# Kernel optimization log

Hardware: AMD Instinct MI355X
Metric: run time of the kernel (lower is better)

Reference implementation:

```python
import jax, jax.numpy as jnp
import numpy as np

S, B, K = 1024, 16, 1024
QD, KD = 1024, 1024


def setup_inputs() -> dict:
    key = jax.random.key(0)
    k1, k2, k3, k4 = jax.random.split(key, 4)
    queries = jax.random.normal(k1, (S, B, QD), dtype=jnp.float32)
    keys = jax.random.normal(k2, (B, K, KD), dtype=jnp.float32)
    null_mask = jax.random.randint(k3, (B, K), 0, 2).astype(jnp.bool_)
    W_in = jax.random.normal(k4, (KD, QD), dtype=jnp.float32) * 0.02
    return {"queries": queries, "keys": keys, "null_mask": null_mask, "W_in": W_in}


def reference(queries, keys, null_mask, W_in):
    # queries: (S, B, QD); keys: (B, K, KD); null_mask: (B, K); W_in: (KD, QD)
    t_query = jnp.einsum('sbq,dq->sbd', queries, W_in)          # linear_in, no bias
    alpha = jnp.einsum('sbd,bkd->sbk', t_query, keys)           # unscaled bilinear scores
    alpha = jnp.where(null_mask[None, :, :], -jnp.inf, alpha)   # masked_fill_
    att_weight = jax.nn.softmax(alpha, axis=2)                  # (S, B, K)
    attened_keys = jnp.einsum('sbk,bkd->sbd', att_weight, keys) # (S, B, KD)
    return (attened_keys, alpha)
```

## Files before the change

### kernel.cpp

```cpp
#include <hip/hip_runtime.h>
#include <math.h>

#define S_DIM 1024
#define B_DIM 16
#define K_DIM 1024
#define QD_DIM 1024
#define KD_DIM 1024
#define MASK_NEG (-3.0e38f)

using short4v = __attribute__((ext_vector_type(4))) short;
using short8v = __attribute__((ext_vector_type(8))) short;
using float4v = __attribute__((ext_vector_type(4))) float;

constexpr int TILE = 128;
constexpr int BK   = 32;
constexpr int LDK  = 36;

#define MFMA(a, b, c) __builtin_amdgcn_mfma_f32_16x16x32_bf16(a, b, c, 0, 0, 0)

__device__ inline void split4(const float4 v, uint2& hi, uint2& lo) {
    uint ax = __float_as_uint(v.x), ay = __float_as_uint(v.y);
    uint az = __float_as_uint(v.z), aw = __float_as_uint(v.w);
    hi.x = __builtin_amdgcn_perm(ay, ax, 0x07060302u);
    hi.y = __builtin_amdgcn_perm(aw, az, 0x07060302u);
    float rx = v.x - __uint_as_float(ax & 0xFFFF0000u);
    float ry = v.y - __uint_as_float(ay & 0xFFFF0000u);
    float rz = v.z - __uint_as_float(az & 0xFFFF0000u);
    float rw = v.w - __uint_as_float(aw & 0xFFFF0000u);
    lo.x = __builtin_amdgcn_perm(__float_as_uint(ry), __float_as_uint(rx), 0x07060302u);
    lo.y = __builtin_amdgcn_perm(__float_as_uint(rw), __float_as_uint(rz), 0x07060302u);
}

__device__ inline short8v frag_load(const short* base) {
    short4v a = *(const short4v*)base;
    short4v b = *(const short4v*)(base + 4);
    return __builtin_shufflevector(a, b, 0, 1, 2, 3, 4, 5, 6, 7);
}

__global__ __launch_bounds__(256) void g1_mfma(const float* __restrict__ Q,
                                               const float* __restrict__ W,
                                               float* __restrict__ TQ) {
    __shared__ short Ah[TILE * LDK], Al[TILE * LDK], Bh[TILE * LDK], Bl[TILE * LDK];
    const int t = threadIdx.x;
    const int lane = t & 63, w = t >> 6;
    const int wm = w >> 1, wn = w & 1;
    const int quad = lane >> 4, l15 = lane & 15;
    const int m0 = blockIdx.y * TILE, n0 = blockIdx.x * TILE;
    const int sr = t >> 3;
    const int sc = (t & 7) * 4;

    float4v acc[4][4] = {};

    for (int k0 = 0; k0 < QD_DIM; k0 += BK) {
        #pragma unroll
        for (int i = 0; i < 4; ++i) {
            const int r = sr + i * 32;
            uint2 h, l;
            float4 va = *(const float4*)(Q + (size_t)(m0 + r) * QD_DIM + k0 + sc);
            split4(va, h, l);
            *(uint2*)&Ah[r * LDK + sc] = h;
            *(uint2*)&Al[r * LDK + sc] = l;
            float4 vb = *(const float4*)(W + (size_t)(n0 + r) * QD_DIM + k0 + sc);
            split4(vb, h, l);
            *(uint2*)&Bh[r * LDK + sc] = h;
            *(uint2*)&Bl[r * LDK + sc] = l;
        }
        __syncthreads();
        short8v ah[4], al[4];
        #pragma unroll
        for (int mt = 0; mt < 4; ++mt) {
            const int ar = (wm * 64 + mt * 16 + l15) * LDK + quad * 8;
            ah[mt] = frag_load(&Ah[ar]);
            al[mt] = frag_load(&Al[ar]);
        }
        #pragma unroll
        for (int nt = 0; nt < 4; ++nt) {
            const int br = (wn * 64 + nt * 16 + l15) * LDK + quad * 8;
            short8v bh = frag_load(&Bh[br]);
            short8v bl = frag_load(&Bl[br]);
            #pragma unroll
            for (int mt = 0; mt < 4; ++mt) acc[mt][nt] = MFMA(ah[mt], bh, acc[mt][nt]);
            #pragma unroll
            for (int mt = 0; mt < 4; ++mt) acc[mt][nt] = MFMA(al[mt], bh, acc[mt][nt]);
            #pragma unroll
            for (int mt = 0; mt < 4; ++mt) acc[mt][nt] = MFMA(ah[mt], bl, acc[mt][nt]);
        }
        __syncthreads();
    }
    #pragma unroll
    for (int mt = 0; mt < 4; ++mt)
        #pragma unroll
        for (int reg = 0; reg < 4; ++reg) {
            const int m = m0 + wm * 64 + mt * 16 + quad * 4 + reg;
            #pragma unroll
            for (int nt = 0; nt < 4; ++nt) {
                const int n = n0 + wn * 64 + nt * 16 + l15;
                TQ[(size_t)m * KD_DIM + n] = acc[mt][nt][reg];
            }
        }
}

__global__ __launch_bounds__(256) void g2_mfma(const float* __restrict__ TQ,
                                               const float* __restrict__ keys,
                                               const int* __restrict__ mask,
                                               float* __restrict__ alpha) {
    __shared__ short Ah[TILE * LDK], Al[TILE * LDK], Bh[TILE * LDK], Bl[TILE * LDK];
    const int t = threadIdx.x;
    const int lane = t & 63, w = t >> 6;
    const int wm = w >> 1, wn = w & 1;
    const int quad = lane >> 4, l15 = lane & 15;
    const int m0 = blockIdx.y * TILE, n0 = blockIdx.x * TILE;
    const int b = blockIdx.z;
    const int sr = t >> 3;
    const int sc = (t & 7) * 4;

    const float* Kb = keys + (size_t)b * K_DIM * KD_DIM;

    float4v acc[4][4] = {};

    for (int k0 = 0; k0 < KD_DIM; k0 += BK) {
        #pragma unroll
        for (int i = 0; i < 4; ++i) {
            const int r = sr + i * 32;
            uint2 h, l;
            float4 va = *(const float4*)(TQ + ((size_t)(m0 + r) * B_DIM + b) * QD_DIM + k0 + sc);
            split4(va, h, l);
            *(uint2*)&Ah[r * LDK + sc] = h;
            *(uint2*)&Al[r * LDK + sc] = l;
            float4 vb = *(const float4*)(Kb + (size_t)(n0 + r) * KD_DIM + k0 + sc);
            split4(vb, h, l);
            *(uint2*)&Bh[r * LDK + sc] = h;
            *(uint2*)&Bl[r * LDK + sc] = l;
        }
        __syncthreads();
        short8v ah[4], al[4];
        #pragma unroll
        for (int mt = 0; mt < 4; ++mt) {
            const int ar = (wm * 64 + mt * 16 + l15) * LDK + quad * 8;
            ah[mt] = frag_load(&Ah[ar]);
            al[mt] = frag_load(&Al[ar]);
        }
        #pragma unroll
        for (int nt = 0; nt < 4; ++nt) {
            const int br = (wn * 64 + nt * 16 + l15) * LDK + quad * 8;
            short8v bh = frag_load(&Bh[br]);
            short8v bl = frag_load(&Bl[br]);
            #pragma unroll
            for (int mt = 0; mt < 4; ++mt) acc[mt][nt] = MFMA(ah[mt], bh, acc[mt][nt]);
            #pragma unroll
            for (int mt = 0; mt < 4; ++mt) acc[mt][nt] = MFMA(al[mt], bh, acc[mt][nt]);
            #pragma unroll
            for (int mt = 0; mt < 4; ++mt) acc[mt][nt] = MFMA(ah[mt], bl, acc[mt][nt]);
        }
        __syncthreads();
    }
    int mk[4];
    #pragma unroll
    for (int nt = 0; nt < 4; ++nt)
        mk[nt] = mask[b * K_DIM + n0 + wn * 64 + nt * 16 + l15];
    #pragma unroll
    for (int mt = 0; mt < 4; ++mt)
        #pragma unroll
        for (int reg = 0; reg < 4; ++reg) {
            const int m = m0 + wm * 64 + mt * 16 + quad * 4 + reg;
            #pragma unroll
            for (int nt = 0; nt < 4; ++nt) {
                const int n = n0 + wn * 64 + nt * 16 + l15;
                alpha[((size_t)m * B_DIM + b) * K_DIM + n] = mk[nt] ? MASK_NEG : acc[mt][nt][reg];
            }
        }
}

__global__ __launch_bounds__(256) void k_stats(const float* __restrict__ alpha,
                                               float* __restrict__ mx,
                                               float* __restrict__ il) {
    const int r = blockIdx.x;
    const int t = threadIdx.x;
    const float4 v = ((const float4*)(alpha + (size_t)r * K_DIM))[t];
    float m = fmaxf(fmaxf(v.x, v.y), fmaxf(v.z, v.w));
    #pragma unroll
    for (int o = 1; o < 64; o <<= 1) m = fmaxf(m, __shfl_xor(m, o, 64));
    __shared__ float redm[4];
    __shared__ float reds[4];
    const int wid = t >> 6;
    if ((t & 63) == 0) redm[wid] = m;
    __syncthreads();
    const float M = fmaxf(fmaxf(redm[0], redm[1]), fmaxf(redm[2], redm[3]));
    float s = expf(v.x - M) + expf(v.y - M) + expf(v.z - M) + expf(v.w - M);
    #pragma unroll
    for (int o = 1; o < 64; o <<= 1) s += __shfl_xor(s, o, 64);
    if ((t & 63) == 0) reds[wid] = s;
    __syncthreads();
    if (t == 0) {
        mx[r] = M;
        il[r] = 1.0f / (reds[0] + reds[1] + reds[2] + reds[3]);
    }
}

__global__ __launch_bounds__(256) void g3_mfma(const float* __restrict__ alpha,
                                               const float* __restrict__ keys,
                                               const float* __restrict__ mx,
                                               const float* __restrict__ il,
                                               float* __restrict__ outk) {
    __shared__ short Ah[TILE * LDK], Al[TILE * LDK], Bh[TILE * LDK], Bl[TILE * LDK];
    __shared__ float Ms[TILE], Ls[TILE];
    const int t = threadIdx.x;
    const int lane = t & 63, w = t >> 6;
    const int wm = w >> 1, wn = w & 1;
    const int quad = lane >> 4, l15 = lane & 15;
    const int m0 = blockIdx.y * TILE, n0 = blockIdx.x * TILE;
    const int b = blockIdx.z;
    const int sr = t >> 3;
    const int sc = (t & 7) * 4;

    const float* Kb = keys + (size_t)b * K_DIM * KD_DIM;

    if (t < TILE) {
        Ms[t] = mx[(size_t)(m0 + t) * B_DIM + b];
        Ls[t] = il[(size_t)(m0 + t) * B_DIM + b];
    }
    __syncthreads();

    float4v acc[4][4] = {};

    for (int k0 = 0; k0 < K_DIM; k0 += BK) {
        #pragma unroll
        for (int i = 0; i < 4; ++i) {
            const int r = sr + i * 32;
            float4 va = *(const float4*)(alpha + ((size_t)(m0 + r) * B_DIM + b) * K_DIM + k0 + sc);
            const float Mv = Ms[r], Lv = Ls[r];
            float4 p;
            p.x = __expf(va.x - Mv) * Lv;
            p.y = __expf(va.y - Mv) * Lv;
            p.z = __expf(va.z - Mv) * Lv;
            p.w = __expf(va.w - Mv) * Lv;
            uint2 h, l;
            split4(p, h, l);
            *(uint2*)&Ah[r * LDK + sc] = h;
            *(uint2*)&Al[r * LDK + sc] = l;
        }
        {
            const int kb = (t >> 5) * 4;
            const int dc = (t & 31) * 4;
            float4 f[4];
            #pragma unroll
            for (int i = 0; i < 4; ++i)
                f[i] = *(const float4*)(Kb + (size_t)(k0 + kb + i) * KD_DIM + n0 + dc);
            #pragma unroll
            for (int e = 0; e < 4; ++e) {
                float4 g;
                g.x = (&f[0].x)[e]; g.y = (&f[1].x)[e];
                g.z = (&f[2].x)[e]; g.w = (&f[3].x)[e];
                uint2 h, l;
                split4(g, h, l);
                *(uint2*)&Bh[(dc + e) * LDK + kb] = h;
                *(uint2*)&Bl[(dc + e) * LDK + kb] = l;
            }
        }
        __syncthreads();
        short8v ah[4], al[4];
        #pragma unroll
        for (int mt = 0; mt < 4; ++mt) {
            const int ar = (wm * 64 + mt * 16 + l15) * LDK + quad * 8;
            ah[mt] = frag_load(&Ah[ar]);
            al[mt] = frag_load(&Al[ar]);
        }
        #pragma unroll
        for (int nt = 0; nt < 4; ++nt) {
            const int br = (wn * 64 + nt * 16 + l15) * LDK + quad * 8;
            short8v bh = frag_load(&Bh[br]);
            short8v bl = frag_load(&Bl[br]);
            #pragma unroll
            for (int mt = 0; mt < 4; ++mt) acc[mt][nt] = MFMA(ah[mt], bh, acc[mt][nt]);
            #pragma unroll
            for (int mt = 0; mt < 4; ++mt) acc[mt][nt] = MFMA(al[mt], bh, acc[mt][nt]);
            #pragma unroll
            for (int mt = 0; mt < 4; ++mt) acc[mt][nt] = MFMA(ah[mt], bl, acc[mt][nt]);
        }
        __syncthreads();
    }
    #pragma unroll
    for (int mt = 0; mt < 4; ++mt)
        #pragma unroll
        for (int reg = 0; reg < 4; ++reg) {
            const int m = m0 + wm * 64 + mt * 16 + quad * 4 + reg;
            #pragma unroll
            for (int nt = 0; nt < 4; ++nt) {
                const int n = n0 + wn * 64 + nt * 16 + l15;
                outk[((size_t)m * B_DIM + b) * KD_DIM + n] = acc[mt][nt][reg];
            }
        }
}

extern "C" void kernel_launch(void* const* d_in, const int* in_sizes, int n_in,
                              void* d_out, int out_size, void* d_ws, size_t ws_size,
                              hipStream_t stream) {
    const float* queries = (const float*)d_in[0];
    const float* keys    = (const float*)d_in[1];
    const int*   mask    = (const int*)d_in[2];
    const float* W_in    = (const float*)d_in[3];

    float* out_attened = (float*)d_out;
    float* out_alpha   = (float*)d_out + (size_t)S_DIM * B_DIM * KD_DIM;

    float* tq = (float*)d_ws;
    float* mx = tq + (size_t)S_DIM * B_DIM * QD_DIM;
    float* il = mx + (size_t)S_DIM * B_DIM;

    dim3 blk(256);

    dim3 grid1(KD_DIM / TILE, (S_DIM * B_DIM) / TILE);
    g1_mfma<<<grid1, blk, 0, stream>>>(queries, W_in, tq);

    dim3 grid2(K_DIM / TILE, S_DIM / TILE, B_DIM);
    g2_mfma<<<grid2, blk, 0, stream>>>(tq, keys, mask, out_alpha);

    k_stats<<<dim3(S_DIM * B_DIM), blk, 0, stream>>>(out_alpha, mx, il);

    dim3 grid3(KD_DIM / TILE, S_DIM / TILE, B_DIM);
    g3_mfma<<<grid3, blk, 0, stream>>>(out_alpha, keys, mx, il, out_attened);
}
```

Baseline: 604.9 us.

## Pre-split operands into bf16 hi/lo planes and stage tiles via global_load_lds

Adds pre-pass kernels that split W and keys into bf16 high/low planes, plus a transposed split copy of keys. The first GEMM now writes its output directly as hi/lo planes in a per-batch layout. The GEMMs then stage these tiles straight into LDS with global_load_lds instead of splitting fp32 values per tile, which removes repeated split work and the strided transpose inside g3. In exchange there are extra launches, more workspace traffic, and a fallback that reuses the output buffers as scratch and needs a final copy when workspace is small. It also drops the LDS padding, which risks bank conflicts.

```diff
diff --git a/kernel.cpp b/kernel.cpp
--- a/kernel.cpp
+++ b/kernel.cpp
@@ -8,17 +8,19 @@
 #define KD_DIM 1024
 #define MASK_NEG (-3.0e38f)
 
-using short4v = __attribute__((ext_vector_type(4))) short;
 using short8v = __attribute__((ext_vector_type(8))) short;
 using float4v = __attribute__((ext_vector_type(4))) float;
 
-constexpr int TILE = 128;
-constexpr int BK   = 32;
-constexpr int LDK  = 36;
-
 #define MFMA(a, b, c) __builtin_amdgcn_mfma_f32_16x16x32_bf16(a, b, c, 0, 0, 0)
 
-__device__ inline void split4(const float4 v, uint2& hi, uint2& lo) {
+
+__device__ __forceinline__ void gll16(const void* g, void* l) {
+    __builtin_amdgcn_global_load_lds((const __attribute__((address_space(1))) unsigned int*)g,
+                                     (__attribute__((address_space(3))) unsigned int*)l,
+                                     16, 0, 0);
+}
+
+__device__ __forceinline__ void split4(const float4 v, uint2& hi, uint2& lo) {
     uint ax = __float_as_uint(v.x), ay = __float_as_uint(v.y);
     uint az = __float_as_uint(v.z), aw = __float_as_uint(v.w);
     hi.x = __builtin_amdgcn_perm(ay, ax, 0x07060302u);
@@ -31,60 +33,91 @@
     lo.y = __builtin_amdgcn_perm(__float_as_uint(rw), __float_as_uint(rz), 0x07060302u);
 }
 
-__device__ inline short8v frag_load(const short* base) {
-    short4v a = *(const short4v*)base;
-    short4v b = *(const short4v*)(base + 4);
-    return __builtin_shufflevector(a, b, 0, 1, 2, 3, 4, 5, 6, 7);
-}
-
-__global__ __launch_bounds__(256) void g1_mfma(const float* __restrict__ Q,
-                                               const float* __restrict__ W,
-                                               float* __restrict__ TQ) {
-    __shared__ short Ah[TILE * LDK], Al[TILE * LDK], Bh[TILE * LDK], Bl[TILE * LDK];
+__device__ __forceinline__ void stage_tile(const short* __restrict__ gplane, int row0, int k0,
+                                           short* lds, int w, int lane) {
+    const short* g0 = gplane + (size_t)(row0 + w * 32 + (lane >> 2)) * 1024 + k0 + (lane & 3) * 8;
+    gll16(g0, lds + w * 1024);
+    gll16(g0 + 16 * 1024, lds + w * 1024 + 512);
+}
+
+__device__ __forceinline__ void mfma_step(const short* __restrict__ Ah, const short* __restrict__ Al,
+                                          const short* __restrict__ Bh, const short* __restrict__ Bl,
+                                          int wm, int wn, int quad, int l15, float4v (&acc)[4][4]) {
+    short8v ah[4], al[4];
+    #pragma unroll
+    for (int mt = 0; mt < 4; ++mt) {
+        const int off = (wm * 64 + mt * 16 + l15) * 32 + quad * 8;
+        ah[mt] = *(const short8v*)(Ah + off);
+        al[mt] = *(const short8v*)(Al + off);
+    }
+    #pragma unroll
+    for (int nt = 0; nt < 4; ++nt) {
+        const int off = (wn * 64 + nt * 16 + l15) * 32 + quad * 8;
+        short8v bh = *(const short8v*)(Bh + off);
+        short8v bl = *(const short8v*)(Bl + off);
+        #pragma unroll
+        for (int mt = 0; mt < 4; ++mt) acc[mt][nt] = MFMA(ah[mt], bh, acc[mt][nt]);
+        #pragma unroll
+        for (int mt = 0; mt < 4; ++mt) acc[mt][nt] = MFMA(al[mt], bh, acc[mt][nt]);
+        #pragma unroll
+        for (int mt = 0; mt < 4; ++mt) acc[mt][nt] = MFMA(ah[mt], bl, acc[mt][nt]);
+    }
+}
+
+__global__ __launch_bounds__(256) void k_split(const float* __restrict__ src,
+                                               short* __restrict__ h, short* __restrict__ l) {
+    const size_t base = ((size_t)blockIdx.x * 256 + threadIdx.x) * 4;
+    const float4 v = *(const float4*)(src + base);
+    uint2 hh, ll;
+    split4(v, hh, ll);
+    *(uint2*)(h + base) = hh;
+    *(uint2*)(l + base) = ll;
+}
+
+__global__ __launch_bounds__(256) void k_transpose(const float* __restrict__ keys,
+                                                   short* __restrict__ th, short* __restrict__ tl) {
+    __shared__ float T[32][33];
     const int t = threadIdx.x;
-    const int lane = t & 63, w = t >> 6;
-    const int wm = w >> 1, wn = w & 1;
-    const int quad = lane >> 4, l15 = lane & 15;
-    const int m0 = blockIdx.y * TILE, n0 = blockIdx.x * TILE;
-    const int sr = t >> 3;
-    const int sc = (t & 7) * 4;
+    const int b = blockIdx.z, d0 = blockIdx.x * 32, k0 = blockIdx.y * 32;
+    const float* Kb = keys + (size_t)b * K_DIM * KD_DIM;
+    const int ry = t >> 3, cx = (t & 7) * 4;
+    const float4 v = *(const float4*)(Kb + (size_t)(k0 + ry) * KD_DIM + d0 + cx);
+    T[ry][cx] = v.x; T[ry][cx + 1] = v.y; T[ry][cx + 2] = v.z; T[ry][cx + 3] = v.w;
+    __syncthreads();
+    float4 g;
+    g.x = T[cx][ry]; g.y = T[cx + 1][ry]; g.z = T[cx + 2][ry]; g.w = T[cx + 3][ry];
+    uint2 hh, ll;
+    split4(g, hh, ll);
+    const size_t o = (size_t)b * K_DIM * KD_DIM + (size_t)(d0 + ry) * K_DIM + k0 + cx;
+    *(uint2*)(th + o) = hh;
+    *(uint2*)(tl + o) = ll;
+}
+
+__global__ __launch_bounds__(256) void g1k(const float* __restrict__ Q,
+                                           const short* __restrict__ Wh, const short* __restrict__ Wl,
+                                           short* __restrict__ TQh, short* __restrict__ TQl) {
+    __shared__ __align__(16) short Ah[128 * 32], Al[128 * 32], Bh[128 * 32], Bl[128 * 32];
+    const int t = threadIdx.x, lane = t & 63, w = t >> 6;
+    const int wm = w >> 1, wn = w & 1, quad = lane >> 4, l15 = lane & 15;
+    const int m0 = blockIdx.y * 128, n0 = blockIdx.x * 128;
+    const int sr = t >> 3, sc = (t & 7) * 4;
 
     float4v acc[4][4] = {};
 
-    for (int k0 = 0; k0 < QD_DIM; k0 += BK) {
+    for (int k0 = 0; k0 < QD_DIM; k0 += 32) {
+        stage_tile(Wh, n0, k0, Bh, w, lane);
+        stage_tile(Wl, n0, k0, Bl, w, lane);
         #pragma unroll
         for (int i = 0; i < 4; ++i) {
             const int r = sr + i * 32;
+            const float4 va = *(const float4*)(Q + (size_t)(m0 + r) * QD_DIM + k0 + sc);
             uint2 h, l;
-            float4 va = *(const float4*)(Q + (size_t)(m0 + r) * QD_DIM + k0 + sc);
             split4(va, h, l);
-            *(uint2*)&Ah[r * LDK + sc] = h;
-            *(uint2*)&Al[r * LDK + sc] = l;
-            float4 vb = *(const float4*)(W + (size_t)(n0 + r) * QD_DIM + k0 + sc);
-            split4(vb, h, l);
-            *(uint2*)&Bh[r * LDK + sc] = h;
-            *(uint2*)&Bl[r * LDK + sc] = l;
-        }
-        __syncthreads();
-        short8v ah[4], al[4];
-        #pragma unroll
-        for (int mt = 0; mt < 4; ++mt) {
-            const int ar = (wm * 64 + mt * 16 + l15) * LDK + quad * 8;
-            ah[mt] = frag_load(&Ah[ar]);
-            al[mt] = frag_load(&Al[ar]);
-        }
-        #pragma unroll
-        for (int nt = 0; nt < 4; ++nt) {
-            const int br = (wn * 64 + nt * 16 + l15) * LDK + quad * 8;
-            short8v bh = frag_load(&Bh[br]);
-            short8v bl = frag_load(&Bl[br]);
-            #pragma unroll
-            for (int mt = 0; mt < 4; ++mt) acc[mt][nt] = MFMA(ah[mt], bh, acc[mt][nt]);
-            #pragma unroll
-            for (int mt = 0; mt < 4; ++mt) acc[mt][nt] = MFMA(al[mt], bh, acc[mt][nt]);
-            #pragma unroll
-            for (int mt = 0; mt < 4; ++mt) acc[mt][nt] = MFMA(ah[mt], bl, acc[mt][nt]);
-        }
+            *(uint2*)&Ah[r * 32 + sc] = h;
+            *(uint2*)&Al[r * 32 + sc] = l;
+        }
+        __syncthreads();
+        mfma_step(Ah, Al, Bh, Bl, wm, wn, quad, l15, acc);
         __syncthreads();
     }
     #pragma unroll
@@ -92,66 +125,42 @@
         #pragma unroll
         for (int reg = 0; reg < 4; ++reg) {
             const int m = m0 + wm * 64 + mt * 16 + quad * 4 + reg;
+            const int s = m >> 4, bq = m & 15;
+            short* th = TQh + (size_t)bq * (1024 * 1024) + (size_t)s * 1024;
+            short* tl = TQl + (size_t)bq * (1024 * 1024) + (size_t)s * 1024;
             #pragma unroll
             for (int nt = 0; nt < 4; ++nt) {
                 const int n = n0 + wn * 64 + nt * 16 + l15;
-                TQ[(size_t)m * KD_DIM + n] = acc[mt][nt][reg];
+                const float x = acc[mt][nt][reg];
+                const uint u = __float_as_uint(x);
+                th[n] = (short)(u >> 16);
+                const float r2 = x - __uint_as_float(u & 0xFFFF0000u);
+                tl[n] = (short)(__float_as_uint(r2) >> 16);
             }
         }
 }
 
-__global__ __launch_bounds__(256) void g2_mfma(const float* __restrict__ TQ,
-                                               const float* __restrict__ keys,
-                                               const int* __restrict__ mask,
-                                               float* __restrict__ alpha) {
-    __shared__ short Ah[TILE * LDK], Al[TILE * LDK], Bh[TILE * LDK], Bl[TILE * LDK];
-    const int t = threadIdx.x;
-    const int lane = t & 63, w = t >> 6;
-    const int wm = w >> 1, wn = w & 1;
-    const int quad = lane >> 4, l15 = lane & 15;
-    const int m0 = blockIdx.y * TILE, n0 = blockIdx.x * TILE;
-    const int b = blockIdx.z;
-    const int sr = t >> 3;
-    const int sc = (t & 7) * 4;
-
-    const float* Kb = keys + (size_t)b * K_DIM * KD_DIM;
+__global__ __launch_bounds__(256) void g2k(const short* __restrict__ TQh, const short* __restrict__ TQl,
+                                           const short* __restrict__ Kh, const short* __restrict__ Kl,
+                                           const int* __restrict__ mask, float* __restrict__ alpha) {
+    __shared__ __align__(16) short Ah[128 * 32], Al[128 * 32], Bh[128 * 32], Bl[128 * 32];
+    const int t = threadIdx.x, lane = t & 63, w = t >> 6;
+    const int wm = w >> 1, wn = w & 1, quad = lane >> 4, l15 = lane & 15;
+    const int m0 = blockIdx.y * 128, n0 = blockIdx.x * 128, b = blockIdx.z;
+    const short* Ahp = TQh + (size_t)b * (1024 * 1024);
+    const short* Alp = TQl + (size_t)b * (1024 * 1024);
+    const short* Bhp = Kh + (size_t)b * (1024 * 1024);
+    const short* Blp = Kl + (size_t)b * (1024 * 1024);
 
     float4v acc[4][4] = {};
 
-    for (int k0 = 0; k0 < KD_DIM; k0 += BK) {
-        #pragma unroll
-        for (int i = 0; i < 4; ++i) {
-            const int r = sr + i * 32;
-            uint2 h, l;
-            float4 va = *(const float4*)(TQ + ((size_t)(m0 + r) * B_DIM + b) * QD_DIM + k0 + sc);
-            split4(va, h, l);
-            *(uint2*)&Ah[r * LDK + sc] = h;
-            *(uint2*)&Al[r * LDK + sc] = l;
-            float4 vb = *(const float4*)(Kb + (size_t)(n0 + r) * KD_DIM + k0 + sc);
-            split4(vb, h, l);
-            *(uint2*)&Bh[r * LDK + sc] = h;
-            *(uint2*)&Bl[r * LDK + sc] = l;
-        }
-        __syncthreads();
-        short8v ah[4], al[4];
-        #pragma unroll
-        for (int mt = 0; mt < 4; ++mt) {
-            const int ar = (wm * 64 + mt * 16 + l15) * LDK + quad * 8;
-            ah[mt] = frag_load(&Ah[ar]);
-            al[mt] = frag_load(&Al[ar]);
-        }
-        #pragma unroll
-        for (int nt = 0; nt < 4; ++nt) {
-            const int br = (wn * 64 + nt * 16 + l15) * LDK + quad * 8;
-            short8v bh = frag_load(&Bh[br]);
-            short8v bl = frag_load(&Bl[br]);
-            #pragma unroll
-            for (int mt = 0; mt < 4; ++mt) acc[mt][nt] = MFMA(ah[mt], bh, acc[mt][nt]);
-            #pragma unroll
-            for (int mt = 0; mt < 4; ++mt) acc[mt][nt] = MFMA(al[mt], bh, acc[mt][nt]);
-            #pragma unroll
-            for (int mt = 0; mt < 4; ++mt) acc[mt][nt] = MFMA(ah[mt], bl, acc[mt][nt]);
-        }
+    for (int k0 = 0; k0 < KD_DIM; k0 += 32) {
+        stage_tile(Ahp, m0, k0, Ah, w, lane);
+        stage_tile(Alp, m0, k0, Al, w, lane);
+        stage_tile(Bhp, n0, k0, Bh, w, lane);
+        stage_tile(Blp, n0, k0, Bl, w, lane);
+        __syncthreads();
+        mfma_step(Ah, Al, Bh, Bl, wm, wn, quad, l15, acc);
         __syncthreads();
     }
     int mk[4];
@@ -197,25 +206,20 @@
     }
 }
 
-__global__ __launch_bounds__(256) void g3_mfma(const float* __restrict__ alpha,
-                                               const float* __restrict__ keys,
-                                               const float* __restrict__ mx,
-                                               const float* __restrict__ il,
-                                               float* __restrict__ outk) {
-    __shared__ short Ah[TILE * LDK], Al[TILE * LDK], Bh[TILE * LDK], Bl[TILE * LDK];
-    __shared__ float Ms[TILE], Ls[TILE];
-    const int t = threadIdx.x;
-    const int lane = t & 63, w = t >> 6;
-    const int wm = w >> 1, wn = w & 1;
-    const int quad = lane >> 4, l15 = lane & 15;
-    const int m0 = blockIdx.y * TILE, n0 = blockIdx.x * TILE;
-    const int b = blockIdx.z;
-    const int sr = t >> 3;
-    const int sc = (t & 7) * 4;
-
-    const float* Kb = keys + (size_t)b * K_DIM * KD_DIM;
-
-    if (t < TILE) {
+__global__ __launch_bounds__(256) void g3k(const float* __restrict__ alpha,
+                                           const short* __restrict__ KTh, const short* __restrict__ KTl,
+                                           const float* __restrict__ mx, const float* __restrict__ il,
+                                           float* __restrict__ outk) {
+    __shared__ __align__(16) short Ah[128 * 32], Al[128 * 32], Bh[128 * 32], Bl[128 * 32];
+    __shared__ float Ms[128], Ls[128];
+    const int t = threadIdx.x, lane = t & 63, w = t >> 6;
+    const int wm = w >> 1, wn = w & 1, quad = lane >> 4, l15 = lane & 15;
+    const int m0 = blockIdx.y * 128, n0 = blockIdx.x * 128, b = blockIdx.z;
+    const int sr = t >> 3, sc = (t & 7) * 4;
+    const short* Bhp = KTh + (size_t)b * (1024 * 1024);
+    const short* Blp = KTl + (size_t)b * (1024 * 1024);
+
+    if (t < 128) {
         Ms[t] = mx[(size_t)(m0 + t) * B_DIM + b];
         Ls[t] = il[(size_t)(m0 + t) * B_DIM + b];
     }
@@ -223,11 +227,13 @@
 
     float4v acc[4][4] = {};
 
-    for (int k0 = 0; k0 < K_DIM; k0 += BK) {
+    for (int k0 = 0; k0 < K_DIM; k0 += 32) {
+        stage_tile(Bhp, n0, k0, Bh, w, lane);
+        stage_tile(Blp, n0, k0, Bl, w, lane);
         #pragma unroll
         for (int i = 0; i < 4; ++i) {
             const int r = sr + i * 32;
-            float4 va = *(const float4*)(alpha + ((size_t)(m0 + r) * B_DIM + b) * K_DIM + k0 + sc);
+            const float4 va = *(const float4*)(alpha + ((size_t)(m0 + r) * B_DIM + b) * K_DIM + k0 + sc);
             const float Mv = Ms[r], Lv = Ls[r];
             float4 p;
             p.x = __expf(va.x - Mv) * Lv;
@@ -236,47 +242,11 @@
             p.w = __expf(va.w - Mv) * Lv;
             uint2 h, l;
             split4(p, h, l);
-            *(uint2*)&Ah[r * LDK + sc] = h;
-            *(uint2*)&Al[r * LDK + sc] = l;
-        }
-        {
-            const int kb = (t >> 5) * 4;
-            const int dc = (t & 31) * 4;
-            float4 f[4];
-            #pragma unroll
-            for (int i = 0; i < 4; ++i)
-                f[i] = *(const float4*)(Kb + (size_t)(k0 + kb + i) * KD_DIM + n0 + dc);
-            #pragma unroll
-            for (int e = 0; e < 4; ++e) {
-                float4 g;
-                g.x = (&f[0].x)[e]; g.y = (&f[1].x)[e];
-                g.z = (&f[2].x)[e]; g.w = (&f[3].x)[e];
-                uint2 h, l;
-                split4(g, h, l);
-                *(uint2*)&Bh[(dc + e) * LDK + kb] = h;
-                *(uint2*)&Bl[(dc + e) * LDK + kb] = l;
-            }
-        }
-        __syncthreads();
-        short8v ah[4], al[4];
-        #pragma unroll
-        for (int mt = 0; mt < 4; ++mt) {
-            const int ar = (wm * 64 + mt * 16 + l15) * LDK + quad * 8;
-            ah[mt] = frag_load(&Ah[ar]);
-            al[mt] = frag_load(&Al[ar]);
-        }
-        #pragma unroll
-        for (int nt = 0; nt < 4; ++nt) {
-            const int br = (wn * 64 + nt * 16 + l15) * LDK + quad * 8;
-            short8v bh = frag_load(&Bh[br]);
-            short8v bl = frag_load(&Bl[br]);
-            #pragma unroll
-            for (int mt = 0; mt < 4; ++mt) acc[mt][nt] = MFMA(ah[mt], bh, acc[mt][nt]);
-            #pragma unroll
-            for (int mt = 0; mt < 4; ++mt) acc[mt][nt] = MFMA(al[mt], bh, acc[mt][nt]);
-            #pragma unroll
-            for (int mt = 0; mt < 4; ++mt) acc[mt][nt] = MFMA(ah[mt], bl, acc[mt][nt]);
-        }
+            *(uint2*)&Ah[r * 32 + sc] = h;
+            *(uint2*)&Al[r * 32 + sc] = l;
+        }
+        __syncthreads();
+        mfma_step(Ah, Al, Bh, Bl, wm, wn, quad, l15, acc);
         __syncthreads();
     }
     #pragma unroll
@@ -292,31 +262,74 @@
         }
 }
 
+__global__ __launch_bounds__(256) void k_copy(const float4* __restrict__ src, float4* __restrict__ dst) {
+    const size_t i = (size_t)blockIdx.x * 256 + threadIdx.x;
+    dst[i] = src[i];
+}
+
 extern "C" void kernel_launch(void* const* d_in, const int* in_sizes, int n_in,
                               void* d_out, int out_size, void* d_ws, size_t ws_size,
                               hipStream_t stream) {
-    const float* queries = (const float*)d_in[0];
-    const float* keys    = (const float*)d_in[1];
-    const int*   mask    = (const int*)d_in[2];
-    const float* W_in    = (const float*)d_in[3];
-
-    float* out_attened = (float*)d_out;
-    float* out_alpha   = (float*)d_out + (size_t)S_DIM * B_DIM * KD_DIM;
-
-    float* tq = (float*)d_ws;
-    float* mx = tq + (size_t)S_DIM * B_DIM * QD_DIM;
-    float* il = mx + (size_t)S_DIM * B_DIM;
+    const float* Q    = (const float*)d_in[0];
+    const float* keys = (const float*)d_in[1];
+    const int*   mask = (const int*)d_in[2];
+    const float* W    = (const float*)d_in[3];
+
+    float* out_att   = (float*)d_out;
+    float* out_alpha = out_att + (size_t)S_DIM * B_DIM * KD_DIM;
+
+    const size_t PL     = (size_t)1024 * 1024;
+    const size_t STREAM = (size_t)B_DIM * PL;
+
+    short *Wh, *Wl, *Khs, *Kls, *KTh, *KTl, *TQh, *TQl;
+    float *mx, *il, *g3out;
+    bool small_ws;
+    char* ws = (char*)d_ws;
+
+    if (ws_size >= ((size_t)197 << 20)) {
+        small_ws = false;
+        Wh  = (short*)ws;
+        Wl  = Wh + PL;
+        Khs = Wl + PL;
+        Kls = Khs + STREAM;
+        KTh = Kls + STREAM;
+        KTl = KTh + STREAM;
+        TQh = KTl + STREAM;
+        TQl = TQh + STREAM;
+        mx  = (float*)(TQl + STREAM);
+        il  = mx + S_DIM * B_DIM;
+        g3out = out_att;
+    } else {
+        small_ws = true;
+        TQh = (short*)ws;
+        TQl = TQh + STREAM;
+        mx  = (float*)(TQl + STREAM);
+        il  = mx + S_DIM * B_DIM;
+        Wh  = (short*)out_alpha;
+        Wl  = Wh + PL;
+        Khs = (short*)out_att;
+        Kls = Khs + STREAM;
+        KTh = Khs;
+        KTl = Kls;
+        g3out = (float*)ws;
+    }
 
     dim3 blk(256);
 
-    dim3 grid1(KD_DIM / TILE, (S_DIM * B_DIM) / TILE);
-    g1_mfma<<<grid1, blk, 0, stream>>>(queries, W_in, tq);
-
-    dim3 grid2(K_DIM / TILE, S_DIM / TILE, B_DIM);
-    g2_mfma<<<grid2, blk, 0, stream>>>(tq, keys, mask, out_alpha);
+    k_split<<<dim3(KD_DIM), blk, 0, stream>>>(W, Wh, Wl);
+    k_split<<<dim3(B_DIM * K_DIM), blk, 0, stream>>>(keys, Khs, Kls);
+
+    g1k<<<dim3(KD_DIM / 128, (S_DIM * B_DIM) / 128), blk, 0, stream>>>(Q, Wh, Wl, TQh, TQl);
+
+    g2k<<<dim3(K_DIM / 128, S_DIM / 128, B_DIM), blk, 0, stream>>>(TQh, TQl, Khs, Kls, mask, out_alpha);
+
+    k_transpose<<<dim3(32, 32, B_DIM), blk, 0, stream>>>(keys, KTh, KTl);
 
     k_stats<<<dim3(S_DIM * B_DIM), blk, 0, stream>>>(out_alpha, mx, il);
 
-    dim3 grid3(KD_DIM / TILE, S_DIM / TILE, B_DIM);
-    g3_mfma<<<grid3, blk, 0, stream>>>(out_alpha, keys, mx, il, out_attened);
-}
+    g3k<<<dim3(KD_DIM / 128, S_DIM / 128, B_DIM), blk, 0, stream>>>(out_alpha, KTh, KTl, mx, il, g3out);
+
+    if (small_ws)
+        k_copy<<<dim3((S_DIM * B_DIM * KD_DIM) / (4 * 256)), blk, 0, stream>>>((const float4*)g3out,
+                                                                               (float4*)out_att);
+}
```

After: 631.9 us. 1.04x slower.
